# Performance work log

Hardware: AMD Instinct MI355X
Metric: run time of the kernel (lower is better)

Reference implementation:

```python
import jax, jax.numpy as jnp
import numpy as np

N = 512
E = N * N
H = 64          # hidden_dim
ED = 6          # edge_dim
L = 4           # n_layers
EPS = 1e-5


def _lin(key, fan_in, fan_out):
    k1, k2 = jax.random.split(key)
    w = jax.random.normal(k1, (fan_in, fan_out), jnp.float32) / np.sqrt(fan_in)
    b = jax.random.normal(k2, (fan_out,), jnp.float32) * 0.01
    return w, b


def _lin_stack(key, fan_in, fan_out, n):
    ws, bs = zip(*[_lin(jax.random.fold_in(key, i), fan_in, fan_out) for i in range(n)])
    return jnp.stack(ws), jnp.stack(bs)


def setup_inputs() -> dict:
    key = jax.random.key(0)
    ks = jax.random.split(key, 16)
    idx = jnp.arange(N, dtype=jnp.int32)
    src = jnp.repeat(idx, N)          # x_j source nodes
    dst = jnp.tile(idx, N)            # x_i target nodes (aggregation index)
    edge_index = jnp.stack([src, dst])  # [2, E]
    x = jax.random.normal(ks[0], (N, 6), jnp.float32)
    edge_attr = jax.random.normal(ks[1], (E, ED), jnp.float32)
    enc_w1, enc_b1 = _lin(ks[2], 6, H)
    enc_w2, enc_b2 = _lin(ks[3], H, H)
    att_w1, att_b1 = _lin_stack(ks[4], 2 * H + ED, H, L)   # [L,134,64]
    att_w2, att_b2 = _lin_stack(ks[5], H, 1, L)
    val_w1, val_b1 = _lin_stack(ks[6], H + ED, H, L)       # [L,70,64]
    val_w2, val_b2 = _lin_stack(ks[7], H, H, L)
    upd_w1, upd_b1 = _lin_stack(ks[8], 2 * H, H, L)        # [L,128,64]
    upd_w2, upd_b2 = _lin_stack(ks[9], H, H, L)
    ln_g = jnp.ones((L, H), jnp.float32)
    ln_b = jnp.zeros((L, H), jnp.float32)
    dec_w1, dec_b1 = _lin(ks[10], H, H)
    dec_w2, dec_b2 = _lin(ks[11], H, 1)
    return dict(x=x, edge_attr=edge_attr,
                enc_w1=enc_w1, enc_b1=enc_b1, enc_w2=enc_w2, enc_b2=enc_b2,
                att_w1=att_w1, att_b1=att_b1, att_w2=att_w2, att_b2=att_b2,
                val_w1=val_w1, val_b1=val_b1, val_w2=val_w2, val_b2=val_b2,
                upd_w1=upd_w1, upd_b1=upd_b1, upd_w2=upd_w2, upd_b2=upd_b2,
                ln_g=ln_g, ln_b=ln_b,
                dec_w1=dec_w1, dec_b1=dec_b1, dec_w2=dec_w2, dec_b2=dec_b2,
                edge_index=edge_index)


def reference(x, edge_attr, enc_w1, enc_b1, enc_w2, enc_b2,
              att_w1, att_b1, att_w2, att_b2,
              val_w1, val_b1, val_w2, val_b2,
              upd_w1, upd_b1, upd_w2, upd_b2,
              ln_g, ln_b, dec_w1, dec_b1, dec_w2, dec_b2, edge_index):
    src, dst = edge_index[0], edge_index[1]
    h = jax.nn.relu(x @ enc_w1 + enc_b1) @ enc_w2 + enc_b2  # [N,H]
    for l in range(L):
        hi = h[dst]                           # x_i  [E,H]
        hj = h[src]                           # x_j  [E,H]
        # attention logits: MLP([x_i || x_j || e])
        a_in = jnp.concatenate([hi, hj, edge_attr], axis=-1)   # [E,2H+ED]
        a = jax.nn.leaky_relu(a_in @ att_w1[l] + att_b1[l], 0.2) @ att_w2[l] + att_b2[l]
        a = a[:, 0]                                            # [E]
        # segment softmax over destination index (numerically stable)
        m = jax.ops.segment_max(a, dst, num_segments=N)
        e = jnp.exp(a - m[dst])
        s = jax.ops.segment_sum(e, dst, num_segments=N)
        alpha = e / s[dst]                                     # [E]
        # values: MLP([x_j || e])
        v_in = jnp.concatenate([hj, edge_attr], axis=-1)       # [E,H+ED]
        v = jax.nn.relu(v_in @ val_w1[l] + val_b1[l]) @ val_w2[l] + val_b2[l]
        agg = jax.ops.segment_sum(v * alpha[:, None], dst, num_segments=N)  # [N,H]
        # update + residual + LayerNorm
        u_in = jnp.concatenate([h, agg], axis=-1)              # [N,2H]
        u = jax.nn.relu(u_in @ upd_w1[l] + upd_b1[l]) @ upd_w2[l] + upd_b2[l]
        r = u + h
        mu = jnp.mean(r, axis=-1, keepdims=True)
        var = jnp.mean((r - mu) ** 2, axis=-1, keepdims=True)
        h = ln_g[l] * (r - mu) / jnp.sqrt(var + EPS) + ln_b[l]
    return jax.nn.relu(h @ dec_w1 + dec_b1) @ dec_w2 + dec_b2  # [N,1]
```

## Files before the change

### kernel.cpp

```cpp
#include <hip/hip_runtime.h>
#include <math.h>

#define NN 512
#define HH 64
#define NLAYERS 4
#define LN_EPS 1e-5f


__global__ void k_transpose(const float* __restrict__ ea, float* __restrict__ eat) {
    int t = blockIdx.x * 256 + threadIdx.x;
    int i = t & (NN - 1);
    int j = t >> 9;
    int e = i * NN + j;
#pragma unroll
    for (int k = 0; k < 6; ++k) eat[(size_t)t * 6 + k] = ea[(size_t)e * 6 + k];
}

__global__ void k_encoder(const float* __restrict__ x,
                          const float* __restrict__ ew1, const float* __restrict__ eb1,
                          const float* __restrict__ ew2, const float* __restrict__ eb2,
                          const float* __restrict__ aw1, const float* __restrict__ ab1,
                          const float* __restrict__ wa2, const float* __restrict__ vw1,
                          const float* __restrict__ vb1,
                          float* __restrict__ h, float* __restrict__ Pd,
                          float* __restrict__ Qs, float* __restrict__ Rv,
                          float* __restrict__ Sq) {
    int j = blockIdx.x, d = threadIdx.x;
    __shared__ float xs[6], t1[HH], hs[HH];
    if (d < 6) xs[d] = x[j * 6 + d];
    __syncthreads();
    float z = eb1[d];
#pragma unroll
    for (int k = 0; k < 6; ++k) z += xs[k] * ew1[k * HH + d];
    t1[d] = fmaxf(z, 0.f);
    __syncthreads();
    float z2 = eb2[d];
    for (int k = 0; k < HH; ++k) z2 += t1[k] * ew2[k * HH + d];
    h[j * HH + d] = z2;
    hs[d] = z2;
    __syncthreads();
    float p = ab1[d], q = 0.f, r = vb1[d];
    for (int k = 0; k < HH; ++k) {
        float hv = hs[k];
        p += hv * aw1[k * HH + d];
        q += hv * aw1[(HH + k) * HH + d];
        r += hv * vw1[k * HH + d];
    }
    Pd[j * HH + d] = p;
    Qs[j * HH + d] = q;
    Rv[j * HH + d] = r;
    float sq = q * wa2[d];
#pragma unroll
    for (int o = 32; o; o >>= 1) sq += __shfl_xor(sq, o);
    if (d == 0) Sq[j] = sq;
}

template <bool TRANS>
__launch_bounds__(256)
__global__ void k_edge(const float* __restrict__ easrc,
                       const float* __restrict__ Pd, const float* __restrict__ Qs,
                       const float* __restrict__ Rv, const float* __restrict__ Sq,
                       const float* __restrict__ waE,
                       const float* __restrict__ wa2v,
                       const float* __restrict__ wvE,
                       float* __restrict__ accv) {
    const int j = blockIdx.x;
    const int tid = threadIdx.x;
    const int lane = tid & 63;
    const int w = tid >> 6;
    const int slot = lane >> 3;
    const int dp = lane & 7;
    const int d0 = dp * 8;

    __shared__ __align__(16) float ea_s[NN * 6];
    __shared__ __align__(16) float Sq_s[NN];
    __shared__ float a_s[NN];
    __shared__ float red_m[4], red_s[4];
    __shared__ float accs[4][HH];

    if (TRANS) {
        const float4* s4 = (const float4*)(easrc + (size_t)j * (NN * 6));
        float4* d4 = (float4*)ea_s;
#pragma unroll
        for (int p = 0; p < 3; ++p) d4[tid + 256 * p] = s4[tid + 256 * p];
    } else {
#pragma unroll
        for (int rep = 0; rep < 2; ++rep) {
            int i = tid + rep * 256;
            const float2* s2 = (const float2*)(easrc + ((size_t)i * NN + j) * 6);
            float2 a0 = s2[0], a1 = s2[1], a2 = s2[2];
            ea_s[i * 6 + 0] = a0.x; ea_s[i * 6 + 1] = a0.y;
            ea_s[i * 6 + 2] = a1.x; ea_s[i * 6 + 3] = a1.y;
            ea_s[i * 6 + 4] = a2.x; ea_s[i * 6 + 5] = a2.y;
        }
    }
    if (tid < 128) ((float4*)Sq_s)[tid] = ((const float4*)Sq)[tid];

    float WA[6][8], WV[6][8], wa2raw[8], wa2r[8], pdr[8];
#pragma unroll
    for (int k = 0; k < 6; ++k)
#pragma unroll
        for (int u = 0; u < 8; ++u) {
            WA[k][u] = waE[k * HH + d0 + u];
            WV[k][u] = wvE[k * HH + d0 + u];
        }
#pragma unroll
    for (int u = 0; u < 8; ++u) {
        wa2raw[u] = wa2v[d0 + u];
        pdr[u] = Pd[(size_t)j * HH + d0 + u];
    }
    float w6s[6];
#pragma unroll
    for (int k = 0; k < 6; ++k) {
        float t = 0.f;
#pragma unroll
        for (int u = 0; u < 8; ++u) t += WA[k][u] * wa2raw[u];
        t += __shfl_xor(t, 1);
        t += __shfl_xor(t, 2);
        t += __shfl_xor(t, 4);
        w6s[k] = 0.6f * t;
    }
#pragma unroll
    for (int u = 0; u < 8; ++u) wa2r[u] = 0.4f * wa2raw[u];

    __syncthreads();

    const int ibw = w * 128;
    float lmax = -1e30f;
    for (int it = 0; it < 16; ++it) {
        const int i = ibw + it * 8 + slot;
        const float4* q4 = (const float4*)(Qs + (size_t)i * HH + d0);
        float4 qa = q4[0], qb = q4[1];
        float qv[8] = {qa.x, qa.y, qa.z, qa.w, qb.x, qb.y, qb.z, qb.w};
        float eav[6];
#pragma unroll
        for (int k = 0; k < 6; ++k) eav[k] = ea_s[i * 6 + k];
        float part = 0.f;
#pragma unroll
        for (int u = 0; u < 8; ++u) {
            float z = pdr[u] + qv[u];
#pragma unroll
            for (int k = 0; k < 6; ++k) z += eav[k] * WA[k][u];
            part += fabsf(z) * wa2r[u];
        }
        part += __shfl_xor(part, 1);
        part += __shfl_xor(part, 2);
        part += __shfl_xor(part, 4);
        float lin = 0.6f * Sq_s[i];
#pragma unroll
        for (int k = 0; k < 6; ++k) lin += eav[k] * w6s[k];
        float a = lin + part;
        if (dp == 0) a_s[i] = a;
        lmax = fmaxf(lmax, a);
    }
#pragma unroll
    for (int o = 32; o; o >>= 1) lmax = fmaxf(lmax, __shfl_xor(lmax, o));
    if (lane == 0) red_m[w] = lmax;
    __syncthreads();
    const float m = fmaxf(fmaxf(red_m[0], red_m[1]), fmaxf(red_m[2], red_m[3]));

    float lsum = 0.f;
#pragma unroll
    for (int rep = 0; rep < 2; ++rep) {
        int i = tid + rep * 256;
        float e = expf(a_s[i] - m);
        a_s[i] = e;
        lsum += e;
    }
#pragma unroll
    for (int o = 32; o; o >>= 1) lsum += __shfl_xor(lsum, o);
    if (lane == 0) red_s[w] = lsum;
    __syncthreads();
    const float s = red_s[0] + red_s[1] + red_s[2] + red_s[3];

    float acc[8] = {0.f, 0.f, 0.f, 0.f, 0.f, 0.f, 0.f, 0.f};
    for (int it = 0; it < 16; ++it) {
        const int i = ibw + it * 8 + slot;
        const float4* r4 = (const float4*)(Rv + (size_t)i * HH + d0);
        float4 ra = r4[0], rb = r4[1];
        float rv[8] = {ra.x, ra.y, ra.z, ra.w, rb.x, rb.y, rb.z, rb.w};
        float eav[6];
#pragma unroll
        for (int k = 0; k < 6; ++k) eav[k] = ea_s[i * 6 + k];
        const float wi = a_s[i];
#pragma unroll
        for (int u = 0; u < 8; ++u) {
            float z = rv[u];
#pragma unroll
            for (int k = 0; k < 6; ++k) z += eav[k] * WV[k][u];
            acc[u] += wi * fmaxf(z, 0.f);
        }
    }
#pragma unroll
    for (int u = 0; u < 8; ++u) {
        acc[u] += __shfl_xor(acc[u], 8);
        acc[u] += __shfl_xor(acc[u], 16);
        acc[u] += __shfl_xor(acc[u], 32);
    }
    if (slot == 0) {
#pragma unroll
        for (int u = 0; u < 8; ++u) accs[w][d0 + u] = acc[u];
    }
    __syncthreads();
    if (tid < HH) {
        float tot = (accs[0][tid] + accs[1][tid] + accs[2][tid] + accs[3][tid]) / s;
        accv[(size_t)j * HH + tid] = tot;
    }
}

__launch_bounds__(256)
__global__ void k_node(const float* __restrict__ h_in, const float* __restrict__ accv,
                       const float* __restrict__ wv2, const float* __restrict__ vb2,
                       const float* __restrict__ uw1, const float* __restrict__ ub1,
                       const float* __restrict__ uw2, const float* __restrict__ ub2,
                       const float* __restrict__ lng, const float* __restrict__ lnb,
                       float* __restrict__ h_out,
                       const float* __restrict__ aw1n, const float* __restrict__ ab1n,
                       const float* __restrict__ wa2n, const float* __restrict__ vw1n,
                       const float* __restrict__ vb1n,
                       float* __restrict__ Pd, float* __restrict__ Qs,
                       float* __restrict__ Rv, float* __restrict__ Sq,
                       int do_prep) {
    const int j = blockIdx.x;
    const int tid = threadIdx.x;
    const int d = tid & 63;
    const int w = tid >> 6;
    __shared__ float av[HH], uin[2 * HH], r1[HH], hs[HH];
    __shared__ float part[4][HH], partQ[4][HH], partR[4][HH];

    float hv = h_in[(size_t)j * HH + d];
    if (w == 0) { av[d] = accv[(size_t)j * HH + d]; uin[d] = hv; }
    __syncthreads();

    float p = (w == 0) ? vb2[d] : 0.f;
    for (int k = w * 16; k < w * 16 + 16; ++k) p += av[k] * wv2[k * HH + d];
    part[w][d] = p;
    __syncthreads();
    if (w == 0) uin[HH + d] = part[0][d] + part[1][d] + part[2][d] + part[3][d];
    __syncthreads();

    float t = (w == 0) ? ub1[d] : 0.f;
    for (int c = w * 32; c < w * 32 + 32; ++c) t += uin[c] * uw1[c * HH + d];
    part[w][d] = t;
    __syncthreads();
    if (w == 0) r1[d] = fmaxf(part[0][d] + part[1][d] + part[2][d] + part[3][d], 0.f);
    __syncthreads();

    float u = (w == 0) ? ub2[d] : 0.f;
    for (int k = w * 16; k < w * 16 + 16; ++k) u += r1[k] * uw2[k * HH + d];
    part[w][d] = u;
    __syncthreads();
    float uu = part[0][d] + part[1][d] + part[2][d] + part[3][d];
    float r = uu + hv;
    float sum = r;
#pragma unroll
    for (int o = 32; o; o >>= 1) sum += __shfl_xor(sum, o);
    float mu = sum * (1.f / HH);
    float dr = r - mu;
    float v2 = dr * dr;
#pragma unroll
    for (int o = 32; o; o >>= 1) v2 += __shfl_xor(v2, o);
    float var = v2 * (1.f / HH);
    float hn = lng[d] * dr * (1.f / sqrtf(var + LN_EPS)) + lnb[d];
    if (w == 0) { h_out[(size_t)j * HH + d] = hn; hs[d] = hn; }
    __syncthreads();

    if (do_prep) {
        float pp = (w == 0) ? ab1n[d] : 0.f, qq = 0.f, rr = (w == 0) ? vb1n[d] : 0.f;
        for (int k = w * 16; k < w * 16 + 16; ++k) {
            float hk = hs[k];
            pp += hk * aw1n[k * HH + d];
            qq += hk * aw1n[(HH + k) * HH + d];
            rr += hk * vw1n[k * HH + d];
        }
        part[w][d] = pp; partQ[w][d] = qq; partR[w][d] = rr;
        __syncthreads();
        float qfull = partQ[0][d] + partQ[1][d] + partQ[2][d] + partQ[3][d];
        if (w == 0) {
            Pd[(size_t)j * HH + d] = part[0][d] + part[1][d] + part[2][d] + part[3][d];
            Qs[(size_t)j * HH + d] = qfull;
            Rv[(size_t)j * HH + d] = partR[0][d] + partR[1][d] + partR[2][d] + partR[3][d];
            float sq = qfull * wa2n[d];
#pragma unroll
            for (int o = 32; o; o >>= 1) sq += __shfl_xor(sq, o);
            if (d == 0) Sq[j] = sq;
        }
    }
}

__global__ void k_decoder(const float* __restrict__ h,
                          const float* __restrict__ dw1, const float* __restrict__ db1,
                          const float* __restrict__ dw2, const float* __restrict__ db2,
                          float* __restrict__ out) {
    int j = blockIdx.x, d = threadIdx.x;
    __shared__ float hs[HH];
    hs[d] = h[(size_t)j * HH + d];
    __syncthreads();
    float t = db1[d];
    for (int k = 0; k < HH; ++k) t += hs[k] * dw1[k * HH + d];
    t = fmaxf(t, 0.f);
    float sum = t * dw2[d];
#pragma unroll
    for (int o = 32; o; o >>= 1) sum += __shfl_xor(sum, o);
    if (d == 0) out[j] = sum + db2[0];
}

extern "C" void kernel_launch(void* const* d_in, const int* in_sizes, int n_in,
                              void* d_out, int out_size, void* d_ws, size_t ws_size,
                              hipStream_t stream) {
    const float* x      = (const float*)d_in[0];
    const float* ea     = (const float*)d_in[1];
    const float* enc_w1 = (const float*)d_in[2];
    const float* enc_b1 = (const float*)d_in[3];
    const float* enc_w2 = (const float*)d_in[4];
    const float* enc_b2 = (const float*)d_in[5];
    const float* att_w1 = (const float*)d_in[6];
    const float* att_b1 = (const float*)d_in[7];
    const float* att_w2 = (const float*)d_in[8];
    const float* val_w1 = (const float*)d_in[10];
    const float* val_b1 = (const float*)d_in[11];
    const float* val_w2 = (const float*)d_in[12];
    const float* val_b2 = (const float*)d_in[13];
    const float* upd_w1 = (const float*)d_in[14];
    const float* upd_b1 = (const float*)d_in[15];
    const float* upd_w2 = (const float*)d_in[16];
    const float* upd_b2 = (const float*)d_in[17];
    const float* ln_g   = (const float*)d_in[18];
    const float* ln_b   = (const float*)d_in[19];
    const float* dec_w1 = (const float*)d_in[20];
    const float* dec_b1 = (const float*)d_in[21];
    const float* dec_w2 = (const float*)d_in[22];
    const float* dec_b2 = (const float*)d_in[23];

    const size_t NH = (size_t)NN * HH;
    const size_t need_full = ((size_t)NN * NN * 6 + 6 * NH + NN) * sizeof(float);
    float* ws = (float*)d_ws;
    const bool trans = (ws_size >= need_full);

    float* EAT  = ws;
    float* base = trans ? ws + (size_t)NN * NN * 6 : ws;
    float* h    = base;
    float* Pd   = h + NH;
    float* Qs   = Pd + NH;
    float* Rv   = Qs + NH;
    float* acc  = Rv + NH;
    float* h2   = acc + NH;
    float* Sq   = h2 + NH;

    if (trans) k_transpose<<<(NN * NN) / 256, 256, 0, stream>>>(ea, EAT);
    k_encoder<<<NN, HH, 0, stream>>>(x, enc_w1, enc_b1, enc_w2, enc_b2,
                                     att_w1, att_b1, att_w2, val_w1, val_b1,
                                     h, Pd, Qs, Rv, Sq);

    const float* easrc = trans ? (const float*)EAT : ea;
    const float* hin = h;
    float* hout = h2;
    for (int l = 0; l < NLAYERS; ++l) {
        const float* aw1 = att_w1 + (size_t)l * 134 * HH;
        const float* vw1 = val_w1 + (size_t)l * 70 * HH;
        if (trans)
            k_edge<true><<<NN, 256, 0, stream>>>(easrc, Pd, Qs, Rv, Sq,
                                                 aw1 + 128 * HH, att_w2 + l * HH,
                                                 vw1 + 64 * HH, acc);
        else
            k_edge<false><<<NN, 256, 0, stream>>>(easrc, Pd, Qs, Rv, Sq,
                                                  aw1 + 128 * HH, att_w2 + l * HH,
                                                  vw1 + 64 * HH, acc);
        int np = (l + 1 < NLAYERS) ? (l + 1) : l;
        k_node<<<NN, 256, 0, stream>>>(hin, acc,
                                       val_w2 + (size_t)l * HH * HH, val_b2 + l * HH,
                                       upd_w1 + (size_t)l * 2 * HH * HH, upd_b1 + l * HH,
                                       upd_w2 + (size_t)l * HH * HH, upd_b2 + l * HH,
                                       ln_g + l * HH, ln_b + l * HH,
                                       hout,
                                       att_w1 + (size_t)np * 134 * HH, att_b1 + np * HH,
                                       att_w2 + np * HH,
                                       val_w1 + (size_t)np * 70 * HH, val_b1 + np * HH,
                                       Pd, Qs, Rv, Sq, (l + 1 < NLAYERS) ? 1 : 0);
        float* tmp = (float*)hin; hin = hout; hout = tmp;
    }
    k_decoder<<<NN, HH, 0, stream>>>(hin, dec_w1, dec_b1, dec_w2, dec_b2, (float*)d_out);
}
```

Before: 261.4 us.

## Fuse whole GNN into one cooperative persistent kernel with grid syncs

Replaces the transpose, encoder, per-layer edge/node kernels and the decoder with a single cooperative kernel: one block per destination node that keeps its edge-attribute column and its node state in shared memory across all layers, using grid.sync between layers. This removes about ten kernel launches, the global round trips of h/Pd/acc, and the separate edge-attribute transpose pass. The cost is that all 512 blocks must be co-resident (2 per CU via launch bounds) and grid barriers are added. If the cooperative launch fails, the old multi-kernel path runs, now always transposing.

```diff
diff --git a/kernel.cpp b/kernel.cpp
--- a/kernel.cpp
+++ b/kernel.cpp
@@ -1,10 +1,281 @@
 #include <hip/hip_runtime.h>
+#include <hip/hip_cooperative_groups.h>
 #include <math.h>
+
+namespace cg = cooperative_groups;
 
 #define NN 512
 #define HH 64
 #define NLAYERS 4
 #define LN_EPS 1e-5f
+
+
+struct GnnParams {
+    const float *x, *ea;
+    const float *ew1, *eb1, *ew2, *eb2;
+    const float *aw1, *ab1, *aw2;
+    const float *vw1, *vb1, *vw2, *vb2;
+    const float *uw1, *ub1, *uw2, *ub2;
+    const float *lng, *lnb;
+    const float *dw1, *db1, *dw2, *db2;
+    float *Qs, *Rv, *Sq, *out;
+};
+
+__launch_bounds__(256, 2)
+__global__ void k_fused(GnnParams P) {
+    cg::grid_group grid = cg::this_grid();
+    const int j = blockIdx.x;
+    const int tid = threadIdx.x;
+    const int lane = tid & 63;
+    const int w = tid >> 6;
+    const int slot = lane >> 3;
+    const int dp = lane & 7;
+    const int d0 = dp * 8;
+    const int d = lane;
+
+    __shared__ __align__(16) float ea_s[NN * 6];
+    __shared__ __align__(16) float Sq_s[NN];
+    __shared__ float a_s[NN];
+    __shared__ float hs[HH], pd_s[HH], av[HH], uin[2 * HH], r1[HH];
+    __shared__ float part[4][HH], partQ[4][HH], partR[4][HH];
+    __shared__ float red_m[4], red_s[4];
+    __shared__ float accs[4][HH];
+
+#pragma unroll
+    for (int rep = 0; rep < 2; ++rep) {
+        int i = tid + rep * 256;
+        const float2* s2 = (const float2*)(P.ea + ((size_t)i * NN + j) * 6);
+        float2 a0 = s2[0], a1 = s2[1], a2 = s2[2];
+        ea_s[i * 6 + 0] = a0.x; ea_s[i * 6 + 1] = a0.y;
+        ea_s[i * 6 + 2] = a1.x; ea_s[i * 6 + 3] = a1.y;
+        ea_s[i * 6 + 4] = a2.x; ea_s[i * 6 + 5] = a2.y;
+    }
+
+    if (w == 0) {
+        float z = P.eb1[d];
+#pragma unroll
+        for (int k = 0; k < 6; ++k) z += P.x[j * 6 + k] * P.ew1[k * HH + d];
+        r1[d] = fmaxf(z, 0.f);
+    }
+    __syncthreads();
+    {
+        float z2 = (w == 0) ? P.eb2[d] : 0.f;
+        for (int k = w * 16; k < w * 16 + 16; ++k) z2 += r1[k] * P.ew2[k * HH + d];
+        part[w][d] = z2;
+    }
+    __syncthreads();
+    if (w == 0) hs[d] = part[0][d] + part[1][d] + part[2][d] + part[3][d];
+    __syncthreads();
+
+    auto do_prep = [&](int l) {
+        const float* a1p = P.aw1 + (size_t)l * 134 * HH;
+        const float* v1p = P.vw1 + (size_t)l * 70 * HH;
+        float pp = (w == 0) ? P.ab1[l * HH + d] : 0.f;
+        float qq = 0.f;
+        float rr = (w == 0) ? P.vb1[l * HH + d] : 0.f;
+        for (int k = w * 16; k < w * 16 + 16; ++k) {
+            float hk = hs[k];
+            pp += hk * a1p[k * HH + d];
+            qq += hk * a1p[(HH + k) * HH + d];
+            rr += hk * v1p[k * HH + d];
+        }
+        part[w][d] = pp; partQ[w][d] = qq; partR[w][d] = rr;
+        __syncthreads();
+        if (w == 0) {
+            float qf = partQ[0][d] + partQ[1][d] + partQ[2][d] + partQ[3][d];
+            pd_s[d] = part[0][d] + part[1][d] + part[2][d] + part[3][d];
+            P.Qs[(size_t)j * HH + d] = qf;
+            P.Rv[(size_t)j * HH + d] = partR[0][d] + partR[1][d] + partR[2][d] + partR[3][d];
+            float sq = qf * P.aw2[l * HH + d];
+#pragma unroll
+            for (int o = 32; o; o >>= 1) sq += __shfl_xor(sq, o);
+            if (d == 0) P.Sq[j] = sq;
+        }
+        __syncthreads();
+    };
+
+    do_prep(0);
+    grid.sync();
+
+    for (int l = 0; l < NLAYERS; ++l) {
+        const float* a1p = P.aw1 + (size_t)l * 134 * HH;
+        const float* waE = a1p + 128 * HH;
+        const float* wvE = P.vw1 + (size_t)l * 70 * HH + 64 * HH;
+        const float* wa2v = P.aw2 + l * HH;
+
+        if (tid < 128) ((float4*)Sq_s)[tid] = ((const float4*)P.Sq)[tid];
+        float WA[6][8], wa2raw[8], wa2r[8], pdr[8], w6s[6];
+#pragma unroll
+        for (int k = 0; k < 6; ++k)
+#pragma unroll
+            for (int u = 0; u < 8; ++u) WA[k][u] = waE[k * HH + d0 + u];
+#pragma unroll
+        for (int u = 0; u < 8; ++u) {
+            wa2raw[u] = wa2v[d0 + u];
+            pdr[u] = pd_s[d0 + u];
+        }
+#pragma unroll
+        for (int k = 0; k < 6; ++k) {
+            float t = 0.f;
+#pragma unroll
+            for (int u = 0; u < 8; ++u) t += WA[k][u] * wa2raw[u];
+            t += __shfl_xor(t, 1);
+            t += __shfl_xor(t, 2);
+            t += __shfl_xor(t, 4);
+            w6s[k] = 0.6f * t;
+        }
+#pragma unroll
+        for (int u = 0; u < 8; ++u) wa2r[u] = 0.4f * wa2raw[u];
+        __syncthreads();
+
+        const int ibw = w * 128;
+        float lmax = -1e30f;
+#pragma unroll 2
+        for (int it = 0; it < 16; ++it) {
+            const int i = ibw + it * 8 + slot;
+            const float4* q4 = (const float4*)(P.Qs + (size_t)i * HH + d0);
+            float4 qa = q4[0], qb = q4[1];
+            float qv[8] = {qa.x, qa.y, qa.z, qa.w, qb.x, qb.y, qb.z, qb.w};
+            float eav[6];
+#pragma unroll
+            for (int k = 0; k < 6; ++k) eav[k] = ea_s[i * 6 + k];
+            float p1 = 0.f;
+#pragma unroll
+            for (int u = 0; u < 8; ++u) {
+                float z = pdr[u] + qv[u];
+#pragma unroll
+                for (int k = 0; k < 6; ++k) z += eav[k] * WA[k][u];
+                p1 += fabsf(z) * wa2r[u];
+            }
+            p1 += __shfl_xor(p1, 1);
+            p1 += __shfl_xor(p1, 2);
+            p1 += __shfl_xor(p1, 4);
+            float lin = 0.6f * Sq_s[i];
+#pragma unroll
+            for (int k = 0; k < 6; ++k) lin += eav[k] * w6s[k];
+            float a = lin + p1;
+            if (dp == 0) a_s[i] = a;
+            lmax = fmaxf(lmax, a);
+        }
+#pragma unroll
+        for (int o = 32; o; o >>= 1) lmax = fmaxf(lmax, __shfl_xor(lmax, o));
+        if (lane == 0) red_m[w] = lmax;
+        __syncthreads();
+        const float m = fmaxf(fmaxf(red_m[0], red_m[1]), fmaxf(red_m[2], red_m[3]));
+        float lsum = 0.f;
+#pragma unroll
+        for (int rep = 0; rep < 2; ++rep) {
+            int i = tid + rep * 256;
+            float e = expf(a_s[i] - m);
+            a_s[i] = e;
+            lsum += e;
+        }
+#pragma unroll
+        for (int o = 32; o; o >>= 1) lsum += __shfl_xor(lsum, o);
+        if (lane == 0) red_s[w] = lsum;
+        __syncthreads();
+        const float s = red_s[0] + red_s[1] + red_s[2] + red_s[3];
+
+        float WV[6][8];
+#pragma unroll
+        for (int k = 0; k < 6; ++k)
+#pragma unroll
+            for (int u = 0; u < 8; ++u) WV[k][u] = wvE[k * HH + d0 + u];
+        float acc[8] = {0.f, 0.f, 0.f, 0.f, 0.f, 0.f, 0.f, 0.f};
+#pragma unroll 2
+        for (int it = 0; it < 16; ++it) {
+            const int i = ibw + it * 8 + slot;
+            const float4* r4 = (const float4*)(P.Rv + (size_t)i * HH + d0);
+            float4 ra = r4[0], rb = r4[1];
+            float rv[8] = {ra.x, ra.y, ra.z, ra.w, rb.x, rb.y, rb.z, rb.w};
+            float eav[6];
+#pragma unroll
+            for (int k = 0; k < 6; ++k) eav[k] = ea_s[i * 6 + k];
+            const float wi = a_s[i];
+#pragma unroll
+            for (int u = 0; u < 8; ++u) {
+                float z = rv[u];
+#pragma unroll
+                for (int k = 0; k < 6; ++k) z += eav[k] * WV[k][u];
+                acc[u] += wi * fmaxf(z, 0.f);
+            }
+        }
+#pragma unroll
+        for (int u = 0; u < 8; ++u) {
+            acc[u] += __shfl_xor(acc[u], 8);
+            acc[u] += __shfl_xor(acc[u], 16);
+            acc[u] += __shfl_xor(acc[u], 32);
+        }
+        if (slot == 0) {
+#pragma unroll
+            for (int u = 0; u < 8; ++u) accs[w][d0 + u] = acc[u];
+        }
+        __syncthreads();
+        if (tid < HH) av[tid] = (accs[0][tid] + accs[1][tid] + accs[2][tid] + accs[3][tid]) / s;
+        __syncthreads();
+
+        const float* wv2 = P.vw2 + (size_t)l * HH * HH;
+        const float* uw1 = P.uw1 + (size_t)l * 2 * HH * HH;
+        const float* uw2 = P.uw2 + (size_t)l * HH * HH;
+        float hv = hs[d];
+        if (w == 0) uin[d] = hv;
+        {
+            float p = (w == 0) ? P.vb2[l * HH + d] : 0.f;
+            for (int k = w * 16; k < w * 16 + 16; ++k) p += av[k] * wv2[k * HH + d];
+            part[w][d] = p;
+        }
+        __syncthreads();
+        if (w == 0) uin[HH + d] = part[0][d] + part[1][d] + part[2][d] + part[3][d];
+        __syncthreads();
+        {
+            float t = (w == 0) ? P.ub1[l * HH + d] : 0.f;
+            for (int c = w * 32; c < w * 32 + 32; ++c) t += uin[c] * uw1[c * HH + d];
+            part[w][d] = t;
+        }
+        __syncthreads();
+        if (w == 0) r1[d] = fmaxf(part[0][d] + part[1][d] + part[2][d] + part[3][d], 0.f);
+        __syncthreads();
+        {
+            float u = (w == 0) ? P.ub2[l * HH + d] : 0.f;
+            for (int k = w * 16; k < w * 16 + 16; ++k) u += r1[k] * uw2[k * HH + d];
+            part[w][d] = u;
+        }
+        __syncthreads();
+        float r = part[0][d] + part[1][d] + part[2][d] + part[3][d] + hv;
+        float sum = r;
+#pragma unroll
+        for (int o = 32; o; o >>= 1) sum += __shfl_xor(sum, o);
+        float mu = sum * (1.f / HH);
+        float dr = r - mu;
+        float v2 = dr * dr;
+#pragma unroll
+        for (int o = 32; o; o >>= 1) v2 += __shfl_xor(v2, o);
+        float var = v2 * (1.f / HH);
+        float hn = P.lng[l * HH + d] * dr * (1.f / sqrtf(var + LN_EPS)) + P.lnb[l * HH + d];
+        __syncthreads();
+        if (w == 0) hs[d] = hn;
+        __syncthreads();
+
+        if (l + 1 < NLAYERS) {
+            do_prep(l + 1);
+            grid.sync();
+        }
+    }
+
+    {
+        float t = (w == 0) ? P.db1[d] : 0.f;
+        for (int k = w * 16; k < w * 16 + 16; ++k) t += hs[k] * P.dw1[k * HH + d];
+        part[w][d] = t;
+    }
+    __syncthreads();
+    if (w == 0) {
+        float tt = fmaxf(part[0][d] + part[1][d] + part[2][d] + part[3][d], 0.f);
+        float sum = tt * P.dw2[d];
+#pragma unroll
+        for (int o = 32; o; o >>= 1) sum += __shfl_xor(sum, o);
+        if (d == 0) P.out[j] = sum + P.db2[0];
+    }
+}
 
 
 __global__ void k_transpose(const float* __restrict__ ea, float* __restrict__ eat) {
@@ -55,15 +326,12 @@
     if (d == 0) Sq[j] = sq;
 }
 
-template <bool TRANS>
 __launch_bounds__(256)
-__global__ void k_edge(const float* __restrict__ easrc,
-                       const float* __restrict__ Pd, const float* __restrict__ Qs,
-                       const float* __restrict__ Rv, const float* __restrict__ Sq,
-                       const float* __restrict__ waE,
-                       const float* __restrict__ wa2v,
-                       const float* __restrict__ wvE,
-                       float* __restrict__ accv) {
+__global__ void k_edge_fb(const float* __restrict__ eat,
+                          const float* __restrict__ Pd, const float* __restrict__ Qs,
+                          const float* __restrict__ Rv, const float* __restrict__ Sq,
+                          const float* __restrict__ waE, const float* __restrict__ wa2v,
+                          const float* __restrict__ wvE, float* __restrict__ accv) {
     const int j = blockIdx.x;
     const int tid = threadIdx.x;
     const int lane = tid & 63;
@@ -78,21 +346,11 @@
     __shared__ float red_m[4], red_s[4];
     __shared__ float accs[4][HH];
 
-    if (TRANS) {
-        const float4* s4 = (const float4*)(easrc + (size_t)j * (NN * 6));
+    {
+        const float4* s4 = (const float4*)(eat + (size_t)j * (NN * 6));
         float4* d4 = (float4*)ea_s;
 #pragma unroll
         for (int p = 0; p < 3; ++p) d4[tid + 256 * p] = s4[tid + 256 * p];
-    } else {
-#pragma unroll
-        for (int rep = 0; rep < 2; ++rep) {
-            int i = tid + rep * 256;
-            const float2* s2 = (const float2*)(easrc + ((size_t)i * NN + j) * 6);
-            float2 a0 = s2[0], a1 = s2[1], a2 = s2[2];
-            ea_s[i * 6 + 0] = a0.x; ea_s[i * 6 + 1] = a0.y;
-            ea_s[i * 6 + 2] = a1.x; ea_s[i * 6 + 3] = a1.y;
-            ea_s[i * 6 + 4] = a2.x; ea_s[i * 6 + 5] = a2.y;
-        }
     }
     if (tid < 128) ((float4*)Sq_s)[tid] = ((const float4*)Sq)[tid];
 
@@ -122,7 +380,6 @@
     }
 #pragma unroll
     for (int u = 0; u < 8; ++u) wa2r[u] = 0.4f * wa2raw[u];
-
     __syncthreads();
 
     const int ibw = w * 128;
@@ -158,7 +415,6 @@
     if (lane == 0) red_m[w] = lmax;
     __syncthreads();
     const float m = fmaxf(fmaxf(red_m[0], red_m[1]), fmaxf(red_m[2], red_m[3]));
-
     float lsum = 0.f;
 #pragma unroll
     for (int rep = 0; rep < 2; ++rep) {
@@ -209,18 +465,18 @@
 }
 
 __launch_bounds__(256)
-__global__ void k_node(const float* __restrict__ h_in, const float* __restrict__ accv,
-                       const float* __restrict__ wv2, const float* __restrict__ vb2,
-                       const float* __restrict__ uw1, const float* __restrict__ ub1,
-                       const float* __restrict__ uw2, const float* __restrict__ ub2,
-                       const float* __restrict__ lng, const float* __restrict__ lnb,
-                       float* __restrict__ h_out,
-                       const float* __restrict__ aw1n, const float* __restrict__ ab1n,
-                       const float* __restrict__ wa2n, const float* __restrict__ vw1n,
-                       const float* __restrict__ vb1n,
-                       float* __restrict__ Pd, float* __restrict__ Qs,
-                       float* __restrict__ Rv, float* __restrict__ Sq,
-                       int do_prep) {
+__global__ void k_node_fb(const float* __restrict__ h_in, const float* __restrict__ accv,
+                          const float* __restrict__ wv2, const float* __restrict__ vb2,
+                          const float* __restrict__ uw1, const float* __restrict__ ub1,
+                          const float* __restrict__ uw2, const float* __restrict__ ub2,
+                          const float* __restrict__ lng, const float* __restrict__ lnb,
+                          float* __restrict__ h_out,
+                          const float* __restrict__ aw1n, const float* __restrict__ ab1n,
+                          const float* __restrict__ wa2n, const float* __restrict__ vw1n,
+                          const float* __restrict__ vb1n,
+                          float* __restrict__ Pd, float* __restrict__ Qs,
+                          float* __restrict__ Rv, float* __restrict__ Sq,
+                          int do_prep) {
     const int j = blockIdx.x;
     const int tid = threadIdx.x;
     const int d = tid & 63;
@@ -231,21 +487,18 @@
     float hv = h_in[(size_t)j * HH + d];
     if (w == 0) { av[d] = accv[(size_t)j * HH + d]; uin[d] = hv; }
     __syncthreads();
-
     float p = (w == 0) ? vb2[d] : 0.f;
     for (int k = w * 16; k < w * 16 + 16; ++k) p += av[k] * wv2[k * HH + d];
     part[w][d] = p;
     __syncthreads();
     if (w == 0) uin[HH + d] = part[0][d] + part[1][d] + part[2][d] + part[3][d];
     __syncthreads();
-
     float t = (w == 0) ? ub1[d] : 0.f;
     for (int c = w * 32; c < w * 32 + 32; ++c) t += uin[c] * uw1[c * HH + d];
     part[w][d] = t;
     __syncthreads();
     if (w == 0) r1[d] = fmaxf(part[0][d] + part[1][d] + part[2][d] + part[3][d], 0.f);
     __syncthreads();
-
     float u = (w == 0) ? ub2[d] : 0.f;
     for (int k = w * 16; k < w * 16 + 16; ++k) u += r1[k] * uw2[k * HH + d];
     part[w][d] = u;
@@ -264,7 +517,6 @@
     float hn = lng[d] * dr * (1.f / sqrtf(var + LN_EPS)) + lnb[d];
     if (w == 0) { h_out[(size_t)j * HH + d] = hn; hs[d] = hn; }
     __syncthreads();
-
     if (do_prep) {
         float pp = (w == 0) ? ab1n[d] : 0.f, qq = 0.f, rr = (w == 0) ? vb1n[d] : 0.f;
         for (int k = w * 16; k < w * 16 + 16; ++k) {
@@ -304,6 +556,7 @@
     for (int o = 32; o; o >>= 1) sum += __shfl_xor(sum, o);
     if (d == 0) out[j] = sum + db2[0];
 }
+
 
 extern "C" void kernel_launch(void* const* d_in, const int* in_sizes, int n_in,
                               void* d_out, int out_size, void* d_ws, size_t ws_size,
@@ -333,12 +586,26 @@
     const float* dec_b2 = (const float*)d_in[23];
 
     const size_t NH = (size_t)NN * HH;
-    const size_t need_full = ((size_t)NN * NN * 6 + 6 * NH + NN) * sizeof(float);
     float* ws = (float*)d_ws;
-    const bool trans = (ws_size >= need_full);
+
+    GnnParams P;
+    P.x = x; P.ea = ea;
+    P.ew1 = enc_w1; P.eb1 = enc_b1; P.ew2 = enc_w2; P.eb2 = enc_b2;
+    P.aw1 = att_w1; P.ab1 = att_b1; P.aw2 = att_w2;
+    P.vw1 = val_w1; P.vb1 = val_b1; P.vw2 = val_w2; P.vb2 = val_b2;
+    P.uw1 = upd_w1; P.ub1 = upd_b1; P.uw2 = upd_w2; P.ub2 = upd_b2;
+    P.lng = ln_g;  P.lnb = ln_b;
+    P.dw1 = dec_w1; P.db1 = dec_b1; P.dw2 = dec_w2; P.db2 = dec_b2;
+    P.Qs = ws; P.Rv = ws + NH; P.Sq = ws + 2 * NH;
+    P.out = (float*)d_out;
+
+    void* kargs[] = { (void*)&P };
+    hipError_t rc = hipLaunchCooperativeKernel((const void*)k_fused, dim3(NN), dim3(256),
+                                               kargs, 0, stream);
+    if (rc == hipSuccess) return;
 
     float* EAT  = ws;
-    float* base = trans ? ws + (size_t)NN * NN * 6 : ws;
+    float* base = ws + (size_t)NN * NN * 6;
     float* h    = base;
     float* Pd   = h + NH;
     float* Qs   = Pd + NH;
@@ -347,36 +614,29 @@
     float* h2   = acc + NH;
     float* Sq   = h2 + NH;
 
-    if (trans) k_transpose<<<(NN * NN) / 256, 256, 0, stream>>>(ea, EAT);
+    k_transpose<<<(NN * NN) / 256, 256, 0, stream>>>(ea, EAT);
     k_encoder<<<NN, HH, 0, stream>>>(x, enc_w1, enc_b1, enc_w2, enc_b2,
                                      att_w1, att_b1, att_w2, val_w1, val_b1,
                                      h, Pd, Qs, Rv, Sq);
-
-    const float* easrc = trans ? (const float*)EAT : ea;
     const float* hin = h;
     float* hout = h2;
     for (int l = 0; l < NLAYERS; ++l) {
         const float* aw1 = att_w1 + (size_t)l * 134 * HH;
         const float* vw1 = val_w1 + (size_t)l * 70 * HH;
-        if (trans)
-            k_edge<true><<<NN, 256, 0, stream>>>(easrc, Pd, Qs, Rv, Sq,
-                                                 aw1 + 128 * HH, att_w2 + l * HH,
-                                                 vw1 + 64 * HH, acc);
-        else
-            k_edge<false><<<NN, 256, 0, stream>>>(easrc, Pd, Qs, Rv, Sq,
-                                                  aw1 + 128 * HH, att_w2 + l * HH,
-                                                  vw1 + 64 * HH, acc);
+        k_edge_fb<<<NN, 256, 0, stream>>>(EAT, Pd, Qs, Rv, Sq,
+                                          aw1 + 128 * HH, att_w2 + l * HH,
+                                          vw1 + 64 * HH, acc);
         int np = (l + 1 < NLAYERS) ? (l + 1) : l;
-        k_node<<<NN, 256, 0, stream>>>(hin, acc,
-                                       val_w2 + (size_t)l * HH * HH, val_b2 + l * HH,
-                                       upd_w1 + (size_t)l * 2 * HH * HH, upd_b1 + l * HH,
-                                       upd_w2 + (size_t)l * HH * HH, upd_b2 + l * HH,
-                                       ln_g + l * HH, ln_b + l * HH,
-                                       hout,
-                                       att_w1 + (size_t)np * 134 * HH, att_b1 + np * HH,
-                                       att_w2 + np * HH,
-                                       val_w1 + (size_t)np * 70 * HH, val_b1 + np * HH,
-                                       Pd, Qs, Rv, Sq, (l + 1 < NLAYERS) ? 1 : 0);
+        k_node_fb<<<NN, 256, 0, stream>>>(hin, acc,
+                                          val_w2 + (size_t)l * HH * HH, val_b2 + l * HH,
+                                          upd_w1 + (size_t)l * 2 * HH * HH, upd_b1 + l * HH,
+                                          upd_w2 + (size_t)l * HH * HH, upd_b2 + l * HH,
+                                          ln_g + l * HH, ln_b + l * HH,
+                                          hout,
+                                          att_w1 + (size_t)np * 134 * HH, att_b1 + np * HH,
+                                          att_w2 + np * HH,
+                                          val_w1 + (size_t)np * 70 * HH, val_b1 + np * HH,
+                                          Pd, Qs, Rv, Sq, (l + 1 < NLAYERS) ? 1 : 0);
         float* tmp = (float*)hin; hin = hout; hout = tmp;
     }
     k_decoder<<<NN, HH, 0, stream>>>(hin, dec_w1, dec_b1, dec_w2, dec_b2, (float*)d_out);
```

New measurement: 448.8 us. +71.7%, slower.

## Fuse edge and node kernels into one per-layer kernel with double-buffered node state

Applied to the files above, without the earlier changes.

Merges the per-layer edge attention/aggregation kernel and the node update/LayerNorm/next-layer-prep kernel into a single 512-thread kernel. Pd/Qs/Rv/Sq and h are double-buffered so one destination node's block can write next-layer values while others still read the current ones. This halves the per-layer launches and drops the accv round trip through global memory. It also widens the encoder and decoder to 256 threads with split-K partial sums, and removes the fallback path that ran without the transposed edge_attr buffer. The cost is a larger workspace requirement and higher register/LDS pressure per block.

```diff
diff --git a/kernel.cpp b/kernel.cpp
--- a/kernel.cpp
+++ b/kernel.cpp
@@ -16,6 +16,7 @@
     for (int k = 0; k < 6; ++k) eat[(size_t)t * 6 + k] = ea[(size_t)e * 6 + k];
 }
 
+__launch_bounds__(256)
 __global__ void k_encoder(const float* __restrict__ x,
                           const float* __restrict__ ew1, const float* __restrict__ eb1,
                           const float* __restrict__ ew2, const float* __restrict__ eb2,
@@ -25,45 +26,75 @@
                           float* __restrict__ h, float* __restrict__ Pd,
                           float* __restrict__ Qs, float* __restrict__ Rv,
                           float* __restrict__ Sq) {
-    int j = blockIdx.x, d = threadIdx.x;
-    __shared__ float xs[6], t1[HH], hs[HH];
-    if (d < 6) xs[d] = x[j * 6 + d];
-    __syncthreads();
-    float z = eb1[d];
-#pragma unroll
-    for (int k = 0; k < 6; ++k) z += xs[k] * ew1[k * HH + d];
-    t1[d] = fmaxf(z, 0.f);
-    __syncthreads();
-    float z2 = eb2[d];
-    for (int k = 0; k < HH; ++k) z2 += t1[k] * ew2[k * HH + d];
-    h[j * HH + d] = z2;
-    hs[d] = z2;
-    __syncthreads();
-    float p = ab1[d], q = 0.f, r = vb1[d];
-    for (int k = 0; k < HH; ++k) {
-        float hv = hs[k];
-        p += hv * aw1[k * HH + d];
-        q += hv * aw1[(HH + k) * HH + d];
-        r += hv * vw1[k * HH + d];
-    }
-    Pd[j * HH + d] = p;
-    Qs[j * HH + d] = q;
-    Rv[j * HH + d] = r;
-    float sq = q * wa2[d];
-#pragma unroll
-    for (int o = 32; o; o >>= 1) sq += __shfl_xor(sq, o);
-    if (d == 0) Sq[j] = sq;
+    const int j = blockIdx.x;
+    const int tid = threadIdx.x;
+    const int d = tid & 63;
+    const int w = tid >> 6;
+    __shared__ float r1[HH], hs[HH];
+    __shared__ float part[4][HH], partQ[4][HH], partR[4][HH];
+
+    if (w == 0) {
+        float z = eb1[d];
+#pragma unroll
+        for (int k = 0; k < 6; ++k) z += x[j * 6 + k] * ew1[k * HH + d];
+        r1[d] = fmaxf(z, 0.f);
+    }
+    __syncthreads();
+    {
+        float z2 = (w == 0) ? eb2[d] : 0.f;
+        for (int k = w * 16; k < w * 16 + 16; ++k) z2 += r1[k] * ew2[k * HH + d];
+        part[w][d] = z2;
+    }
+    __syncthreads();
+    if (w == 0) {
+        float hv = part[0][d] + part[1][d] + part[2][d] + part[3][d];
+        h[(size_t)j * HH + d] = hv;
+        hs[d] = hv;
+    }
+    __syncthreads();
+    {
+        float pp = (w == 0) ? ab1[d] : 0.f;
+        float qq = 0.f;
+        float rr = (w == 0) ? vb1[d] : 0.f;
+        for (int k = w * 16; k < w * 16 + 16; ++k) {
+            float hk = hs[k];
+            pp += hk * aw1[k * HH + d];
+            qq += hk * aw1[(HH + k) * HH + d];
+            rr += hk * vw1[k * HH + d];
+        }
+        part[w][d] = pp; partQ[w][d] = qq; partR[w][d] = rr;
+    }
+    __syncthreads();
+    if (w == 0) {
+        float qf = partQ[0][d] + partQ[1][d] + partQ[2][d] + partQ[3][d];
+        Pd[(size_t)j * HH + d] = part[0][d] + part[1][d] + part[2][d] + part[3][d];
+        Qs[(size_t)j * HH + d] = qf;
+        Rv[(size_t)j * HH + d] = partR[0][d] + partR[1][d] + partR[2][d] + partR[3][d];
+        float sq = qf * wa2[d];
+#pragma unroll
+        for (int o = 32; o; o >>= 1) sq += __shfl_xor(sq, o);
+        if (d == 0) Sq[j] = sq;
+    }
 }
 
-template <bool TRANS>
-__launch_bounds__(256)
-__global__ void k_edge(const float* __restrict__ easrc,
-                       const float* __restrict__ Pd, const float* __restrict__ Qs,
-                       const float* __restrict__ Rv, const float* __restrict__ Sq,
-                       const float* __restrict__ waE,
-                       const float* __restrict__ wa2v,
-                       const float* __restrict__ wvE,
-                       float* __restrict__ accv) {
+__launch_bounds__(512, 4)
+__global__ void k_layer(const float* __restrict__ eat, const float* __restrict__ h_in,
+                        const float* __restrict__ Pd, const float* __restrict__ Qs,
+                        const float* __restrict__ Rv, const float* __restrict__ Sq,
+                        const float* __restrict__ waE,
+                        const float* __restrict__ wa2v,
+                        const float* __restrict__ wvE,
+                        const float* __restrict__ wv2, const float* __restrict__ vb2,
+                        const float* __restrict__ uw1, const float* __restrict__ ub1,
+                        const float* __restrict__ uw2, const float* __restrict__ ub2,
+                        const float* __restrict__ lng, const float* __restrict__ lnb,
+                        float* __restrict__ h_out,
+                        const float* __restrict__ aw1n, const float* __restrict__ ab1n,
+                        const float* __restrict__ wa2n, const float* __restrict__ vw1n,
+                        const float* __restrict__ vb1n,
+                        float* __restrict__ Pdn, float* __restrict__ Qsn,
+                        float* __restrict__ Rvn, float* __restrict__ Sqn,
+                        int do_prep) {
     const int j = blockIdx.x;
     const int tid = threadIdx.x;
     const int lane = tid & 63;
@@ -71,45 +102,34 @@
     const int slot = lane >> 3;
     const int dp = lane & 7;
     const int d0 = dp * 8;
+    const int d = lane;
 
     __shared__ __align__(16) float ea_s[NN * 6];
     __shared__ __align__(16) float Sq_s[NN];
     __shared__ float a_s[NN];
-    __shared__ float red_m[4], red_s[4];
-    __shared__ float accs[4][HH];
-
-    if (TRANS) {
-        const float4* s4 = (const float4*)(easrc + (size_t)j * (NN * 6));
+    __shared__ float red_m[8], red_s[8];
+    __shared__ float accs[8][HH];
+    __shared__ float av[HH], uin[2 * HH], r1[HH], hs[HH];
+    __shared__ float part[8][HH], partQ[8][HH], partR[8][HH];
+
+    {
+        const float4* s4 = (const float4*)(eat + (size_t)j * (NN * 6));
         float4* d4 = (float4*)ea_s;
-#pragma unroll
-        for (int p = 0; p < 3; ++p) d4[tid + 256 * p] = s4[tid + 256 * p];
-    } else {
-#pragma unroll
-        for (int rep = 0; rep < 2; ++rep) {
-            int i = tid + rep * 256;
-            const float2* s2 = (const float2*)(easrc + ((size_t)i * NN + j) * 6);
-            float2 a0 = s2[0], a1 = s2[1], a2 = s2[2];
-            ea_s[i * 6 + 0] = a0.x; ea_s[i * 6 + 1] = a0.y;
-            ea_s[i * 6 + 2] = a1.x; ea_s[i * 6 + 3] = a1.y;
-            ea_s[i * 6 + 4] = a2.x; ea_s[i * 6 + 5] = a2.y;
-        }
+        d4[tid] = s4[tid];
+        if (tid < 256) d4[tid + 512] = s4[tid + 512];
     }
     if (tid < 128) ((float4*)Sq_s)[tid] = ((const float4*)Sq)[tid];
 
-    float WA[6][8], WV[6][8], wa2raw[8], wa2r[8], pdr[8];
+    float WA[6][8], wa2raw[8], wa2r[8], pdr[8], w6s[6];
 #pragma unroll
     for (int k = 0; k < 6; ++k)
 #pragma unroll
-        for (int u = 0; u < 8; ++u) {
-            WA[k][u] = waE[k * HH + d0 + u];
-            WV[k][u] = wvE[k * HH + d0 + u];
-        }
+        for (int u = 0; u < 8; ++u) WA[k][u] = waE[k * HH + d0 + u];
 #pragma unroll
     for (int u = 0; u < 8; ++u) {
         wa2raw[u] = wa2v[d0 + u];
         pdr[u] = Pd[(size_t)j * HH + d0 + u];
     }
-    float w6s[6];
 #pragma unroll
     for (int k = 0; k < 6; ++k) {
         float t = 0.f;
@@ -122,12 +142,12 @@
     }
 #pragma unroll
     for (int u = 0; u < 8; ++u) wa2r[u] = 0.4f * wa2raw[u];
-
-    __syncthreads();
-
-    const int ibw = w * 128;
+    __syncthreads();
+
+    const int ibw = w * 64;
     float lmax = -1e30f;
-    for (int it = 0; it < 16; ++it) {
+#pragma unroll
+    for (int it = 0; it < 8; ++it) {
         const int i = ibw + it * 8 + slot;
         const float4* q4 = (const float4*)(Qs + (size_t)i * HH + d0);
         float4 qa = q4[0], qb = q4[1];
@@ -135,21 +155,21 @@
         float eav[6];
 #pragma unroll
         for (int k = 0; k < 6; ++k) eav[k] = ea_s[i * 6 + k];
-        float part = 0.f;
+        float p1 = 0.f;
 #pragma unroll
         for (int u = 0; u < 8; ++u) {
             float z = pdr[u] + qv[u];
 #pragma unroll
             for (int k = 0; k < 6; ++k) z += eav[k] * WA[k][u];
-            part += fabsf(z) * wa2r[u];
+            p1 += fabsf(z) * wa2r[u];
         }
-        part += __shfl_xor(part, 1);
-        part += __shfl_xor(part, 2);
-        part += __shfl_xor(part, 4);
+        p1 += __shfl_xor(p1, 1);
+        p1 += __shfl_xor(p1, 2);
+        p1 += __shfl_xor(p1, 4);
         float lin = 0.6f * Sq_s[i];
 #pragma unroll
         for (int k = 0; k < 6; ++k) lin += eav[k] * w6s[k];
-        float a = lin + part;
+        float a = lin + p1;
         if (dp == 0) a_s[i] = a;
         lmax = fmaxf(lmax, a);
     }
@@ -157,24 +177,29 @@
     for (int o = 32; o; o >>= 1) lmax = fmaxf(lmax, __shfl_xor(lmax, o));
     if (lane == 0) red_m[w] = lmax;
     __syncthreads();
-    const float m = fmaxf(fmaxf(red_m[0], red_m[1]), fmaxf(red_m[2], red_m[3]));
-
-    float lsum = 0.f;
-#pragma unroll
-    for (int rep = 0; rep < 2; ++rep) {
-        int i = tid + rep * 256;
-        float e = expf(a_s[i] - m);
-        a_s[i] = e;
-        lsum += e;
-    }
+    float m = red_m[0];
+#pragma unroll
+    for (int q = 1; q < 8; ++q) m = fmaxf(m, red_m[q]);
+
+    float e = expf(a_s[tid] - m);
+    a_s[tid] = e;
+    float lsum = e;
 #pragma unroll
     for (int o = 32; o; o >>= 1) lsum += __shfl_xor(lsum, o);
     if (lane == 0) red_s[w] = lsum;
     __syncthreads();
-    const float s = red_s[0] + red_s[1] + red_s[2] + red_s[3];
-
+    float s = red_s[0];
+#pragma unroll
+    for (int q = 1; q < 8; ++q) s += red_s[q];
+
+    float WV[6][8];
+#pragma unroll
+    for (int k = 0; k < 6; ++k)
+#pragma unroll
+        for (int u = 0; u < 8; ++u) WV[k][u] = wvE[k * HH + d0 + u];
     float acc[8] = {0.f, 0.f, 0.f, 0.f, 0.f, 0.f, 0.f, 0.f};
-    for (int it = 0; it < 16; ++it) {
+#pragma unroll
+    for (int it = 0; it < 8; ++it) {
         const int i = ibw + it * 8 + slot;
         const float4* r4 = (const float4*)(Rv + (size_t)i * HH + d0);
         float4 ra = r4[0], rb = r4[1];
@@ -203,71 +228,71 @@
     }
     __syncthreads();
     if (tid < HH) {
-        float tot = (accs[0][tid] + accs[1][tid] + accs[2][tid] + accs[3][tid]) / s;
-        accv[(size_t)j * HH + tid] = tot;
-    }
-}
-
-__launch_bounds__(256)
-__global__ void k_node(const float* __restrict__ h_in, const float* __restrict__ accv,
-                       const float* __restrict__ wv2, const float* __restrict__ vb2,
-                       const float* __restrict__ uw1, const float* __restrict__ ub1,
-                       const float* __restrict__ uw2, const float* __restrict__ ub2,
-                       const float* __restrict__ lng, const float* __restrict__ lnb,
-                       float* __restrict__ h_out,
-                       const float* __restrict__ aw1n, const float* __restrict__ ab1n,
-                       const float* __restrict__ wa2n, const float* __restrict__ vw1n,
-                       const float* __restrict__ vb1n,
-                       float* __restrict__ Pd, float* __restrict__ Qs,
-                       float* __restrict__ Rv, float* __restrict__ Sq,
-                       int do_prep) {
-    const int j = blockIdx.x;
-    const int tid = threadIdx.x;
-    const int d = tid & 63;
-    const int w = tid >> 6;
-    __shared__ float av[HH], uin[2 * HH], r1[HH], hs[HH];
-    __shared__ float part[4][HH], partQ[4][HH], partR[4][HH];
-
-    float hv = h_in[(size_t)j * HH + d];
-    if (w == 0) { av[d] = accv[(size_t)j * HH + d]; uin[d] = hv; }
-    __syncthreads();
-
-    float p = (w == 0) ? vb2[d] : 0.f;
-    for (int k = w * 16; k < w * 16 + 16; ++k) p += av[k] * wv2[k * HH + d];
-    part[w][d] = p;
-    __syncthreads();
-    if (w == 0) uin[HH + d] = part[0][d] + part[1][d] + part[2][d] + part[3][d];
-    __syncthreads();
-
-    float t = (w == 0) ? ub1[d] : 0.f;
-    for (int c = w * 32; c < w * 32 + 32; ++c) t += uin[c] * uw1[c * HH + d];
-    part[w][d] = t;
-    __syncthreads();
-    if (w == 0) r1[d] = fmaxf(part[0][d] + part[1][d] + part[2][d] + part[3][d], 0.f);
-    __syncthreads();
-
-    float u = (w == 0) ? ub2[d] : 0.f;
-    for (int k = w * 16; k < w * 16 + 16; ++k) u += r1[k] * uw2[k * HH + d];
-    part[w][d] = u;
-    __syncthreads();
-    float uu = part[0][d] + part[1][d] + part[2][d] + part[3][d];
-    float r = uu + hv;
-    float sum = r;
-#pragma unroll
-    for (int o = 32; o; o >>= 1) sum += __shfl_xor(sum, o);
-    float mu = sum * (1.f / HH);
-    float dr = r - mu;
-    float v2 = dr * dr;
-#pragma unroll
-    for (int o = 32; o; o >>= 1) v2 += __shfl_xor(v2, o);
-    float var = v2 * (1.f / HH);
-    float hn = lng[d] * dr * (1.f / sqrtf(var + LN_EPS)) + lnb[d];
-    if (w == 0) { h_out[(size_t)j * HH + d] = hn; hs[d] = hn; }
+        float tot = accs[0][tid];
+#pragma unroll
+        for (int q = 1; q < 8; ++q) tot += accs[q][tid];
+        av[tid] = tot / s;
+    }
+    __syncthreads();
+
+    const float hv = h_in[(size_t)j * HH + d];
+    {
+        float p = (w == 0) ? vb2[d] : 0.f;
+        for (int k = w * 8; k < w * 8 + 8; ++k) p += av[k] * wv2[k * HH + d];
+        part[w][d] = p;
+        if (w == 0) uin[d] = hv;
+    }
+    __syncthreads();
+    if (w == 0) {
+        float agg = part[0][d];
+#pragma unroll
+        for (int q = 1; q < 8; ++q) agg += part[q][d];
+        uin[HH + d] = agg;
+    }
+    __syncthreads();
+    {
+        float t = (w == 0) ? ub1[d] : 0.f;
+        for (int c = w * 16; c < w * 16 + 16; ++c) t += uin[c] * uw1[c * HH + d];
+        part[w][d] = t;
+    }
+    __syncthreads();
+    if (w == 0) {
+        float t = part[0][d];
+#pragma unroll
+        for (int q = 1; q < 8; ++q) t += part[q][d];
+        r1[d] = fmaxf(t, 0.f);
+    }
+    __syncthreads();
+    {
+        float u = (w == 0) ? ub2[d] : 0.f;
+        for (int k = w * 8; k < w * 8 + 8; ++k) u += r1[k] * uw2[k * HH + d];
+        part[w][d] = u;
+    }
+    __syncthreads();
+    if (w == 0) {
+        float r = hv + part[0][d];
+#pragma unroll
+        for (int q = 1; q < 8; ++q) r += part[q][d];
+        float sum = r;
+#pragma unroll
+        for (int o = 32; o; o >>= 1) sum += __shfl_xor(sum, o);
+        float mu = sum * (1.f / HH);
+        float dr = r - mu;
+        float v2 = dr * dr;
+#pragma unroll
+        for (int o = 32; o; o >>= 1) v2 += __shfl_xor(v2, o);
+        float var = v2 * (1.f / HH);
+        float hn = lng[d] * dr * (1.f / sqrtf(var + LN_EPS)) + lnb[d];
+        h_out[(size_t)j * HH + d] = hn;
+        hs[d] = hn;
+    }
     __syncthreads();
 
     if (do_prep) {
-        float pp = (w == 0) ? ab1n[d] : 0.f, qq = 0.f, rr = (w == 0) ? vb1n[d] : 0.f;
-        for (int k = w * 16; k < w * 16 + 16; ++k) {
+        float pp = (w == 0) ? ab1n[d] : 0.f;
+        float qq = 0.f;
+        float rr = (w == 0) ? vb1n[d] : 0.f;
+        for (int k = w * 8; k < w * 8 + 8; ++k) {
             float hk = hs[k];
             pp += hk * aw1n[k * HH + d];
             qq += hk * aw1n[(HH + k) * HH + d];
@@ -275,34 +300,46 @@
         }
         part[w][d] = pp; partQ[w][d] = qq; partR[w][d] = rr;
         __syncthreads();
-        float qfull = partQ[0][d] + partQ[1][d] + partQ[2][d] + partQ[3][d];
         if (w == 0) {
-            Pd[(size_t)j * HH + d] = part[0][d] + part[1][d] + part[2][d] + part[3][d];
-            Qs[(size_t)j * HH + d] = qfull;
-            Rv[(size_t)j * HH + d] = partR[0][d] + partR[1][d] + partR[2][d] + partR[3][d];
-            float sq = qfull * wa2n[d];
+            float pf = part[0][d], qf = partQ[0][d], rf = partR[0][d];
+#pragma unroll
+            for (int q = 1; q < 8; ++q) {
+                pf += part[q][d]; qf += partQ[q][d]; rf += partR[q][d];
+            }
+            Pdn[(size_t)j * HH + d] = pf;
+            Qsn[(size_t)j * HH + d] = qf;
+            Rvn[(size_t)j * HH + d] = rf;
+            float sq = qf * wa2n[d];
 #pragma unroll
             for (int o = 32; o; o >>= 1) sq += __shfl_xor(sq, o);
-            if (d == 0) Sq[j] = sq;
+            if (d == 0) Sqn[j] = sq;
         }
     }
 }
 
+__launch_bounds__(256)
 __global__ void k_decoder(const float* __restrict__ h,
                           const float* __restrict__ dw1, const float* __restrict__ db1,
                           const float* __restrict__ dw2, const float* __restrict__ db2,
                           float* __restrict__ out) {
-    int j = blockIdx.x, d = threadIdx.x;
-    __shared__ float hs[HH];
-    hs[d] = h[(size_t)j * HH + d];
-    __syncthreads();
-    float t = db1[d];
-    for (int k = 0; k < HH; ++k) t += hs[k] * dw1[k * HH + d];
-    t = fmaxf(t, 0.f);
-    float sum = t * dw2[d];
-#pragma unroll
-    for (int o = 32; o; o >>= 1) sum += __shfl_xor(sum, o);
-    if (d == 0) out[j] = sum + db2[0];
+    const int j = blockIdx.x;
+    const int tid = threadIdx.x;
+    const int d = tid & 63;
+    const int w = tid >> 6;
+    __shared__ float hs[HH], part[4][HH];
+    if (w == 0) hs[d] = h[(size_t)j * HH + d];
+    __syncthreads();
+    float t = (w == 0) ? db1[d] : 0.f;
+    for (int k = w * 16; k < w * 16 + 16; ++k) t += hs[k] * dw1[k * HH + d];
+    part[w][d] = t;
+    __syncthreads();
+    if (w == 0) {
+        float tt = fmaxf(part[0][d] + part[1][d] + part[2][d] + part[3][d], 0.f);
+        float sum = tt * dw2[d];
+#pragma unroll
+        for (int o = 32; o; o >>= 1) sum += __shfl_xor(sum, o);
+        if (d == 0) out[j] = sum + db2[0];
+    }
 }
 
 extern "C" void kernel_launch(void* const* d_in, const int* in_sizes, int n_in,
@@ -333,51 +370,49 @@
     const float* dec_b2 = (const float*)d_in[23];
 
     const size_t NH = (size_t)NN * HH;
-    const size_t need_full = ((size_t)NN * NN * 6 + 6 * NH + NN) * sizeof(float);
-    float* ws = (float*)d_ws;
-    const bool trans = (ws_size >= need_full);
-
+    float* ws   = (float*)d_ws;
     float* EAT  = ws;
-    float* base = trans ? ws + (size_t)NN * NN * 6 : ws;
-    float* h    = base;
-    float* Pd   = h + NH;
-    float* Qs   = Pd + NH;
-    float* Rv   = Qs + NH;
-    float* acc  = Rv + NH;
-    float* h2   = acc + NH;
-    float* Sq   = h2 + NH;
-
-    if (trans) k_transpose<<<(NN * NN) / 256, 256, 0, stream>>>(ea, EAT);
-    k_encoder<<<NN, HH, 0, stream>>>(x, enc_w1, enc_b1, enc_w2, enc_b2,
-                                     att_w1, att_b1, att_w2, val_w1, val_b1,
-                                     h, Pd, Qs, Rv, Sq);
-
-    const float* easrc = trans ? (const float*)EAT : ea;
-    const float* hin = h;
-    float* hout = h2;
+    float* h0   = EAT + (size_t)NN * NN * 6;
+    float* h1   = h0 + NH;
+    float* Pd0  = h1 + NH;
+    float* Pd1  = Pd0 + NH;
+    float* Qs0  = Pd1 + NH;
+    float* Qs1  = Qs0 + NH;
+    float* Rv0  = Qs1 + NH;
+    float* Rv1  = Rv0 + NH;
+    float* Sq0  = Rv1 + NH;
+    float* Sq1  = Sq0 + NN;
+
+    float* Pdb[2] = {Pd0, Pd1};
+    float* Qsb[2] = {Qs0, Qs1};
+    float* Rvb[2] = {Rv0, Rv1};
+    float* Sqb[2] = {Sq0, Sq1};
+    float* hb[2]  = {h0, h1};
+
+    k_transpose<<<(NN * NN) / 256, 256, 0, stream>>>(ea, EAT);
+    k_encoder<<<NN, 256, 0, stream>>>(x, enc_w1, enc_b1, enc_w2, enc_b2,
+                                      att_w1, att_b1, att_w2, val_w1, val_b1,
+                                      h0, Pd0, Qs0, Rv0, Sq0);
+
     for (int l = 0; l < NLAYERS; ++l) {
+        const int cur = l & 1, nxt = (l + 1) & 1;
+        const int np = (l + 1 < NLAYERS) ? (l + 1) : l;
         const float* aw1 = att_w1 + (size_t)l * 134 * HH;
         const float* vw1 = val_w1 + (size_t)l * 70 * HH;
-        if (trans)
-            k_edge<true><<<NN, 256, 0, stream>>>(easrc, Pd, Qs, Rv, Sq,
-                                                 aw1 + 128 * HH, att_w2 + l * HH,
-                                                 vw1 + 64 * HH, acc);
-        else
-            k_edge<false><<<NN, 256, 0, stream>>>(easrc, Pd, Qs, Rv, Sq,
-                                                  aw1 + 128 * HH, att_w2 + l * HH,
-                                                  vw1 + 64 * HH, acc);
-        int np = (l + 1 < NLAYERS) ? (l + 1) : l;
-        k_node<<<NN, 256, 0, stream>>>(hin, acc,
-                                       val_w2 + (size_t)l * HH * HH, val_b2 + l * HH,
-                                       upd_w1 + (size_t)l * 2 * HH * HH, upd_b1 + l * HH,
-                                       upd_w2 + (size_t)l * HH * HH, upd_b2 + l * HH,
-                                       ln_g + l * HH, ln_b + l * HH,
-                                       hout,
-                                       att_w1 + (size_t)np * 134 * HH, att_b1 + np * HH,
-                                       att_w2 + np * HH,
-                                       val_w1 + (size_t)np * 70 * HH, val_b1 + np * HH,
-                                       Pd, Qs, Rv, Sq, (l + 1 < NLAYERS) ? 1 : 0);
-        float* tmp = (float*)hin; hin = hout; hout = tmp;
-    }
-    k_decoder<<<NN, HH, 0, stream>>>(hin, dec_w1, dec_b1, dec_w2, dec_b2, (float*)d_out);
+        k_layer<<<NN, 512, 0, stream>>>(
+            EAT, hb[cur],
+            Pdb[cur], Qsb[cur], Rvb[cur], Sqb[cur],
+            aw1 + 128 * HH, att_w2 + l * HH, vw1 + 64 * HH,
+            val_w2 + (size_t)l * HH * HH, val_b2 + l * HH,
+            upd_w1 + (size_t)l * 2 * HH * HH, upd_b1 + l * HH,
+            upd_w2 + (size_t)l * HH * HH, upd_b2 + l * HH,
+            ln_g + l * HH, ln_b + l * HH,
+            hb[nxt],
+            att_w1 + (size_t)np * 134 * HH, att_b1 + np * HH, att_w2 + np * HH,
+            val_w1 + (size_t)np * 70 * HH, val_b1 + np * HH,
+            Pdb[nxt], Qsb[nxt], Rvb[nxt], Sqb[nxt],
+            (l + 1 < NLAYERS) ? 1 : 0);
+    }
+    k_decoder<<<NN, 256, 0, stream>>>(hb[NLAYERS & 1], dec_w1, dec_b1, dec_w2, dec_b2,
+                                      (float*)d_out);
 }
```

Measured after the change: 213.3 us. 1.23x faster.
